# Kernel optimization log

Hardware: AMD Instinct MI355X
Metric: run time of the kernel (lower is better)

The kernel has to match this reference:

```python
import jax, jax.numpy as jnp
import numpy as np
from jax import lax

B, C, H, W = 8, 256, 128, 128
NH = 8
HD = C // NH
EPS = 1e-5


def setup_inputs() -> dict:
    key = jax.random.key(0)
    ks = jax.random.split(key, 6)
    x = jax.random.normal(ks[0], (B, C, H, W), dtype=jnp.float32)
    dw_weight = jax.random.normal(ks[1], (C, 1, 3, 3), dtype=jnp.float32) * 0.1
    off_weight = jax.random.normal(ks[2], (NH * 2, C), dtype=jnp.float32) * 0.05
    off_bias = jnp.zeros((NH * 2,), dtype=jnp.float32)
    v_weight = jax.random.normal(ks[3], (C, C), dtype=jnp.float32) * (1.0 / np.sqrt(C))
    o_weight = jax.random.normal(ks[4], (C, C), dtype=jnp.float32) * (1.0 / np.sqrt(C))
    gamma = jnp.ones((C,), dtype=jnp.float32)
    beta = jnp.zeros((C,), dtype=jnp.float32)
    return {"x": x, "dw_weight": dw_weight, "off_weight": off_weight, "off_bias": off_bias,
            "v_weight": v_weight, "o_weight": o_weight, "gamma": gamma, "beta": beta}


def reference(x, dw_weight, off_weight, off_bias, v_weight, o_weight, gamma, beta):
    b, c, h, w = x.shape
    # --- offset branch: depthwise 3x3 + pointwise 1x1 ---
    hdw = lax.conv_general_dilated(x, dw_weight, (1, 1), 'SAME',
                                   feature_group_count=c,
                                   dimension_numbers=('NCHW', 'OIHW', 'NCHW'))
    offsets = jnp.einsum('bchw,oc->bohw', hdw, off_weight) + off_bias[None, :, None, None]
    offsets = jnp.tanh(offsets) * 0.5                      # (B, 2*NH, H, W)
    offsets = offsets.reshape(b, NH, 2, h, w)
    dy, dx = offsets[:, :, 0], offsets[:, :, 1]            # (B, NH, H, W)

    # --- value projection, split into heads ---
    V = jnp.einsum('bchw,oc->bohw', x, v_weight).reshape(b, NH, HD, h, w)

    # --- deformable bilinear sampling (grid_sample, align_corners=True, border pad) ---
    gy = jnp.linspace(-1.0, 1.0, h, dtype=x.dtype)[None, None, :, None]
    gx = jnp.linspace(-1.0, 1.0, w, dtype=x.dtype)[None, None, None, :]
    sx = jnp.clip(gx + dx, -1.0, 1.0)                      # (B, NH, H, W)
    sy = jnp.clip(gy + dy, -1.0, 1.0)
    ix = (sx + 1.0) * 0.5 * (w - 1)                        # unnormalized coords
    iy = (sy + 1.0) * 0.5 * (h - 1)
    x0f = jnp.floor(ix); y0f = jnp.floor(iy)
    wx = ix - x0f; wy = iy - y0f
    x0 = jnp.clip(x0f.astype(jnp.int32), 0, w - 1)
    x1 = jnp.clip(x0f.astype(jnp.int32) + 1, 0, w - 1)
    y0 = jnp.clip(y0f.astype(jnp.int32), 0, h - 1)
    y1 = jnp.clip(y0f.astype(jnp.int32) + 1, 0, h - 1)

    Vf = V.reshape(b, NH, HD, h * w)

    def gather(yi, xi):
        idx = (yi * w + xi).reshape(b, NH, 1, h * w)
        return jnp.take_along_axis(Vf, idx, axis=3)        # (B, NH, HD, H*W)

    wx_ = wx.reshape(b, NH, 1, h * w); wy_ = wy.reshape(b, NH, 1, h * w)
    sampled = (gather(y0, x0) * (1 - wx_) * (1 - wy_)
               + gather(y0, x1) * wx_ * (1 - wy_)
               + gather(y1, x0) * (1 - wx_) * wy_
               + gather(y1, x1) * wx_ * wy_)
    out = sampled.reshape(b, c, h, w)

    # --- output projection + GroupNorm(NH groups) + residual ---
    out = jnp.einsum('bchw,oc->bohw', out, o_weight)
    g = out.reshape(b, NH, HD * h * w)
    mu = jnp.mean(g, axis=-1, keepdims=True)
    var = jnp.mean(jnp.square(g - mu), axis=-1, keepdims=True)
    g = (g - mu) * lax.rsqrt(var + EPS)
    out = g.reshape(b, c, h, w) * gamma[None, :, None, None] + beta[None, :, None, None]
    return x + out
```

## Files before the change

kernel.cpp:

```cpp
#include <hip/hip_runtime.h>
#include <hip/hip_bf16.h>

#define B_ 8
#define C_ 256
#define H_ 128
#define W_ 128
#define HW_ 16384
#define CHW_ (C_ * HW_)
#define NH_ 8
#define HD_ 32
#define NTOT (B_ * CHW_)

typedef short short8 __attribute__((ext_vector_type(8)));
typedef float f32x4 __attribute__((ext_vector_type(4)));

__global__ __launch_bounds__(256) void wconv_kernel(const float* __restrict__ vw,
                                                    const float* __restrict__ ow,
                                                    __hip_bfloat16* __restrict__ wvb,
                                                    __hip_bfloat16* __restrict__ wob) {
    int i = blockIdx.x * 256 + threadIdx.x;
    wvb[i] = __float2bfloat16(vw[i]);
    wob[i] = __float2bfloat16(ow[i]);
}

__global__ __launch_bounds__(256) void xt_kernel(const float* __restrict__ x,
                                                 __hip_bfloat16* __restrict__ xT) {
    __shared__ float tile[64][68];
    int t = threadIdx.x;
    int p0 = blockIdx.x * 64, c0 = blockIdx.y * 64, b = blockIdx.z;
    const float* xb = x + ((size_t)b * C_ + c0) * HW_ + p0;
#pragma unroll
    for (int l = 0; l < 4; ++l) {
        int idx = t + 256 * l;
        int row = idx >> 4, cf = idx & 15;
        float4 v = *(const float4*)&xb[(size_t)row * HW_ + cf * 4];
        *(float4*)&tile[row][cf * 4] = v;
    }
    __syncthreads();
    __hip_bfloat16* op = xT + ((size_t)b * HW_ + p0) * C_ + c0;
#pragma unroll
    for (int l = 0; l < 2; ++l) {
        int idx = t + 256 * l;
        int p = idx & 63, oct = idx >> 6;
        __hip_bfloat16 arr[8];
#pragma unroll
        for (int j = 0; j < 8; ++j) arr[j] = __float2bfloat16(tile[oct * 8 + j][p]);
        *(int4*)(op + (size_t)p * C_ + oct * 8) = *(int4*)arr;
    }
}

__global__ __launch_bounds__(256) void fused_offset_kernel(const float* __restrict__ x,
                                                           const float* __restrict__ dww,
                                                           const float* __restrict__ offw,
                                                           float* __restrict__ partials) {
    __shared__ float xt[4][10][136];
    __shared__ float wT[32][16];
    __shared__ float wd[32][9];
    int t = threadIdx.x;
    int rt = blockIdx.x, cg = blockIdx.y, b = blockIdx.z;
    int h0 = rt * 8, c0 = cg * 32;
    for (int i = t; i < 512; i += 256) { int o = i >> 5, c = i & 31; wT[c][o] = offw[o * 256 + c0 + c]; }
    for (int i = t; i < 288; i += 256) { wd[i / 9][i % 9] = dww[(c0 + i / 9) * 9 + i % 9]; }
    const float* xb = x + ((size_t)b * C_ + c0) * HW_;
    int col = t & 127;
    int sb = (t >> 7) * 4;
    float acc[4][16] = {};
    for (int cc0 = 0; cc0 < 32; cc0 += 4) {
        __syncthreads();
#pragma unroll
        for (int l = 0; l < 5; ++l) {
            int idx = t + 256 * l;
            int pr = idx >> 5, c4 = idx & 31;
            int cc = pr / 10, r = pr - cc * 10;
            int gh = h0 - 1 + r;
            float4 v = make_float4(0.f, 0.f, 0.f, 0.f);
            if (gh >= 0 && gh < H_)
                v = *(const float4*)&xb[(size_t)(cc0 + cc) * HW_ + gh * W_ + c4 * 4];
            *(float4*)&xt[cc][r][4 + c4 * 4] = v;
        }
        if (t < 80) { int pr = t >> 1, side = t & 1; xt[pr / 10][pr % 10][side ? 132 : 3] = 0.f; }
        __syncthreads();
#pragma unroll
        for (int cc = 0; cc < 4; ++cc) {
            float win[6][3];
#pragma unroll
            for (int rr = 0; rr < 6; ++rr)
#pragma unroll
                for (int kk = 0; kk < 3; ++kk)
                    win[rr][kk] = xt[cc][sb + rr][col + 3 + kk];
            float w9[9];
#pragma unroll
            for (int k9 = 0; k9 < 9; ++k9) w9[k9] = wd[cc0 + cc][k9];
#pragma unroll
            for (int j = 0; j < 4; ++j) {
                float s = 0.f;
#pragma unroll
                for (int ky = 0; ky < 3; ++ky)
#pragma unroll
                    for (int kx = 0; kx < 3; ++kx)
                        s += win[j + ky][kx] * w9[ky * 3 + kx];
#pragma unroll
                for (int o = 0; o < 16; ++o) acc[j][o] += s * wT[cc0 + cc][o];
            }
        }
    }
    float* pb = partials + (size_t)(cg * 8 + b) * 16 * HW_;
#pragma unroll
    for (int o = 0; o < 16; ++o)
#pragma unroll
        for (int j = 0; j < 4; ++j)
            pb[(size_t)o * HW_ + (h0 + sb + j) * W_ + col] = acc[j][o];
}

__global__ __launch_bounds__(256) void offreduce_kernel(const float* __restrict__ partials,
                                                        const float* __restrict__ offb,
                                                        float* __restrict__ off_buf) {
    int i = blockIdx.x * 256 + threadIdx.x;
    float s = 0.f;
#pragma unroll
    for (int cg = 0; cg < 8; ++cg) s += partials[(size_t)cg * 2097152 + i];
    int o = (i >> 14) & 15;
    off_buf[i] = tanhf(s + offb[o]) * 0.5f;
}

template<bool TRANS, bool STATS>
__global__ __launch_bounds__(256, 2) void mfma_gemm(const __hip_bfloat16* __restrict__ Wb,
                                                    const __hip_bfloat16* __restrict__ Xt,
                                                    void* __restrict__ Y,
                                                    float* __restrict__ stats) {
    int t = threadIdx.x;
    int wave = t >> 6, lane = t & 63;
    int quad = lane >> 4, l16 = lane & 15;
    int b = blockIdx.z;
    int n0 = blockIdx.x * 128, m0 = blockIdx.y * 128;
    const short* Wp = (const short*)Wb + (size_t)(m0 + wave * 32) * 256;
    const short* Xp = (const short*)Xt + ((size_t)b * HW_ + n0) * 256;

    short8 af[8][2];
#pragma unroll
    for (int ks = 0; ks < 8; ++ks)
#pragma unroll
        for (int mt = 0; mt < 2; ++mt)
            af[ks][mt] = *(const short8*)(Wp + (size_t)(mt * 16 + l16) * 256 + ks * 32 + quad * 8);

    const short* Xl = Xp + (size_t)l16 * 256 + quad * 8;
    short8 bf[3][8];
#pragma unroll
    for (int pf = 0; pf < 2; ++pf)
#pragma unroll
        for (int nt = 0; nt < 8; ++nt)
            bf[pf][nt] = *(const short8*)(Xl + (size_t)nt * 16 * 256 + pf * 32);

    f32x4 acc[2][8];
#pragma unroll
    for (int mt = 0; mt < 2; ++mt)
#pragma unroll
        for (int nt = 0; nt < 8; ++nt) acc[mt][nt] = (f32x4){0.f, 0.f, 0.f, 0.f};

#pragma unroll
    for (int ks = 0; ks < 8; ++ks) {
        if (ks < 6) {
#pragma unroll
            for (int nt = 0; nt < 8; ++nt)
                bf[(ks + 2) % 3][nt] = *(const short8*)(Xl + (size_t)nt * 16 * 256 + (ks + 2) * 32);
        }
#pragma unroll
        for (int mt = 0; mt < 2; ++mt)
#pragma unroll
            for (int nt = 0; nt < 8; ++nt)
                acc[mt][nt] = __builtin_amdgcn_mfma_f32_16x16x32_bf16(af[ks][mt], bf[ks % 3][nt], acc[mt][nt], 0, 0, 0);
    }

    if constexpr (TRANS) {
        __hip_bfloat16* Yb = (__hip_bfloat16*)Y + (size_t)b * CHW_;
#pragma unroll
        for (int mt = 0; mt < 2; ++mt)
#pragma unroll
            for (int nt = 0; nt < 8; ++nt) {
                int m = m0 + wave * 32 + mt * 16 + quad * 4;
                int n = n0 + nt * 16 + l16;
                __hip_bfloat16 arr[4];
#pragma unroll
                for (int r = 0; r < 4; ++r) arr[r] = __float2bfloat16(acc[mt][nt][r]);
                *(int2*)((__hip_bfloat16*)Yb + (size_t)n * C_ + m) = *(int2*)arr;
            }
    } else {
        float* Yb = (float*)Y + (size_t)b * CHW_;
#pragma unroll
        for (int mt = 0; mt < 2; ++mt)
#pragma unroll
            for (int nt = 0; nt < 8; ++nt)
#pragma unroll
                for (int r = 0; r < 4; ++r) {
                    int m = m0 + wave * 32 + mt * 16 + quad * 4 + r;
                    int n = n0 + nt * 16 + l16;
                    Yb[(size_t)m * HW_ + n] = acc[mt][nt][r];
                }
    }
    if constexpr (STATS) {
        float s1 = 0.f, s2 = 0.f;
#pragma unroll
        for (int mt = 0; mt < 2; ++mt)
#pragma unroll
            for (int nt = 0; nt < 8; ++nt)
#pragma unroll
                for (int r = 0; r < 4; ++r) {
                    float v = acc[mt][nt][r];
                    s1 += v;
                    s2 += v * v;
                }
#pragma unroll
        for (int o = 32; o; o >>= 1) {
            s1 += __shfl_down(s1, o);
            s2 += __shfl_down(s2, o);
        }
        if (lane == 0) {
            int grp = b * NH_ + (m0 >> 5) + wave;
            atomicAdd(&stats[grp * 2 + 0], s1);
            atomicAdd(&stats[grp * 2 + 1], s2);
        }
    }
}

__global__ __launch_bounds__(256) void sample_kernel(const __hip_bfloat16* __restrict__ VT,
                                                     const float* __restrict__ off,
                                                     __hip_bfloat16* __restrict__ sT) {
    int t = threadIdx.x;
    int chunk = t & 3;
    int g = t >> 2;
    int head = g & 7;
    int p = blockIdx.x * 8 + (g >> 3);
    int b = blockIdx.z;
    int h = p >> 7, w = p & 127;
    const float* ob = off + ((size_t)b * 16 + head * 2) * HW_ + p;
    float dy = ob[0], dx = ob[HW_];
    float gy = h * (2.0f / 127.0f) - 1.0f;
    float gx = w * (2.0f / 127.0f) - 1.0f;
    float sx = fminf(fmaxf(gx + dx, -1.0f), 1.0f);
    float sy = fminf(fmaxf(gy + dy, -1.0f), 1.0f);
    float ix = (sx + 1.0f) * 0.5f * 127.0f;
    float iy = (sy + 1.0f) * 0.5f * 127.0f;
    float x0f = floorf(ix), y0f = floorf(iy);
    float wx = ix - x0f, wy = iy - y0f;
    int x0 = min(max((int)x0f, 0), 127);
    int x1 = min((int)x0f + 1, 127);
    int y0 = min(max((int)y0f, 0), 127);
    int y1 = min((int)y0f + 1, 127);
    float w00 = (1.f - wx) * (1.f - wy), w01 = wx * (1.f - wy);
    float w10 = (1.f - wx) * wy, w11 = wx * wy;
    const short* Vb = (const short*)VT + (size_t)b * CHW_ + head * 32 + chunk * 8;
    short8 v00 = *(const short8*)(Vb + (size_t)(y0 * W_ + x0) * C_);
    short8 v01 = *(const short8*)(Vb + (size_t)(y0 * W_ + x1) * C_);
    short8 v10 = *(const short8*)(Vb + (size_t)(y1 * W_ + x0) * C_);
    short8 v11 = *(const short8*)(Vb + (size_t)(y1 * W_ + x1) * C_);
    __hip_bfloat16 arr[8];
#pragma unroll
    for (int j = 0; j < 8; ++j) {
        float f = __bfloat162float(((const __hip_bfloat16*)&v00)[j]) * w00 +
                  __bfloat162float(((const __hip_bfloat16*)&v01)[j]) * w01 +
                  __bfloat162float(((const __hip_bfloat16*)&v10)[j]) * w10 +
                  __bfloat162float(((const __hip_bfloat16*)&v11)[j]) * w11;
        arr[j] = __float2bfloat16(f);
    }
    __hip_bfloat16* op = sT + ((size_t)b * HW_ + p) * C_ + head * 32 + chunk * 8;
    *(int4*)op = *(int4*)arr;
}

__global__ __launch_bounds__(256) void final_kernel(const float* __restrict__ x,
                                                    const float* __restrict__ stats,
                                                    const float* __restrict__ gamma,
                                                    const float* __restrict__ beta,
                                                    float* __restrict__ out) {
    int idx = (blockIdx.x * 256 + threadIdx.x) * 4;
    int c = (idx >> 14) & 255;
    int b = idx >> 22;
    int grp = b * NH_ + (c >> 5);
    const float invN = 1.0f / (float)(HD_ * HW_);
    float mu = stats[grp * 2 + 0] * invN;
    float var = stats[grp * 2 + 1] * invN - mu * mu;
    float r = rsqrtf(var + 1e-5f);
    float g = gamma[c], be = beta[c];
    float4 v = *(const float4*)&out[idx];
    float4 xv = *(const float4*)&x[idx];
    float4 o;
    o.x = xv.x + (v.x - mu) * r * g + be;
    o.y = xv.y + (v.y - mu) * r * g + be;
    o.z = xv.z + (v.z - mu) * r * g + be;
    o.w = xv.w + (v.w - mu) * r * g + be;
    *(float4*)&out[idx] = o;
}

extern "C" void kernel_launch(void* const* d_in, const int* in_sizes, int n_in,
                              void* d_out, int out_size, void* d_ws, size_t ws_size,
                              hipStream_t stream) {
    const float* x     = (const float*)d_in[0];
    const float* dww   = (const float*)d_in[1];
    const float* offw  = (const float*)d_in[2];
    const float* offb  = (const float*)d_in[3];
    const float* vw    = (const float*)d_in[4];
    const float* ow    = (const float*)d_in[5];
    const float* gamma = (const float*)d_in[6];
    const float* beta  = (const float*)d_in[7];
    float* out = (float*)d_out;
    float* ws_f = (float*)d_ws;

    float* partials = ws_f;
    float* off_buf  = ws_f + 16777216;
    float* stats    = ws_f + 18874368;
    __hip_bfloat16* wvb = (__hip_bfloat16*)(ws_f + 18874624);
    __hip_bfloat16* wob = wvb + 65536;
    __hip_bfloat16* xT  = (__hip_bfloat16*)(ws_f + 18940160);
    __hip_bfloat16* sT  = (__hip_bfloat16*)partials;
    __hip_bfloat16* vT  = (__hip_bfloat16*)out;

    wconv_kernel<<<256, 256, 0, stream>>>(vw, ow, wvb, wob);
    xt_kernel<<<dim3(256, 4, 8), 256, 0, stream>>>(x, xT);
    fused_offset_kernel<<<dim3(16, 8, 8), 256, 0, stream>>>(x, dww, offw, partials);
    offreduce_kernel<<<8192, 256, 0, stream>>>(partials, offb, off_buf);
    mfma_gemm<true, false><<<dim3(128, 2, 8), 256, 0, stream>>>(wvb, xT, (void*)vT, nullptr);
    sample_kernel<<<dim3(2048, 1, 8), 256, 0, stream>>>(vT, off_buf, sT);
    hipMemsetAsync(stats, 0, 128 * sizeof(float), stream);
    mfma_gemm<false, true><<<dim3(128, 2, 8), 256, 0, stream>>>(wob, sT, (void*)out, stats);
    final_kernel<<<NTOT / 1024, 256, 0, stream>>>(x, stats, gamma, beta, out);
}
```

Before: 641.9 us.

## Stage GEMM tiles through swizzled LDS via global_load_lds with higher occupancy

The MFMA GEMM used to load A and B fragments straight from global memory into registers, with register double-buffering. It now copies 128x32 tiles of each operand into LDS with direct global-to-LDS loads, using an XOR swizzle to avoid bank conflicts. Fragments are then read from LDS, and each k-step is bracketed by barriers. Register use drops, so the launch bound rises to 4 blocks per CU, but the loads are no longer prefetched ahead of the compute and each step waits on two syncthreads.

Result: faster. 572.1 us (-10.9%).

```diff
diff --git a/kernel.cpp b/kernel.cpp
--- a/kernel.cpp
+++ b/kernel.cpp
@@ -124,51 +124,57 @@
 }
 
 template<bool TRANS, bool STATS>
-__global__ __launch_bounds__(256, 2) void mfma_gemm(const __hip_bfloat16* __restrict__ Wb,
+__global__ __launch_bounds__(256, 4) void mfma_gemm(const __hip_bfloat16* __restrict__ Wb,
                                                     const __hip_bfloat16* __restrict__ Xt,
                                                     void* __restrict__ Y,
                                                     float* __restrict__ stats) {
+    __shared__ __align__(16) short As[128 * 32];
+    __shared__ __align__(16) short Bs[128 * 32];
     int t = threadIdx.x;
     int wave = t >> 6, lane = t & 63;
     int quad = lane >> 4, l16 = lane & 15;
     int b = blockIdx.z;
     int n0 = blockIdx.x * 128, m0 = blockIdx.y * 128;
-    const short* Wp = (const short*)Wb + (size_t)(m0 + wave * 32) * 256;
+    const short* Wp = (const short*)Wb + (size_t)m0 * 256;
     const short* Xp = (const short*)Xt + ((size_t)b * HW_ + n0) * 256;
 
-    short8 af[8][2];
-#pragma unroll
-    for (int ks = 0; ks < 8; ++ks)
+    int i0 = t, i1 = t + 256;
+    int r0 = i0 >> 2, r1 = i1 >> 2;
+    int ss0 = (i0 & 3) ^ ((r0 >> 1) & 3);
+    int ss1 = (i1 & 3) ^ ((r1 >> 1) & 3);
+
+    f32x4 acc[2][8];
+#pragma unroll
+    for (int mt = 0; mt < 2; ++mt)
+#pragma unroll
+        for (int nt = 0; nt < 8; ++nt) acc[mt][nt] = (f32x4){0.f, 0.f, 0.f, 0.f};
+
+    for (int kk = 0; kk < 8; ++kk) {
+        int ko = kk * 32;
+        __builtin_amdgcn_global_load_lds(Wp + (size_t)r0 * 256 + ko + ss0 * 8, &As[i0 * 8], 16, 0, 0);
+        __builtin_amdgcn_global_load_lds(Wp + (size_t)r1 * 256 + ko + ss1 * 8, &As[i1 * 8], 16, 0, 0);
+        __builtin_amdgcn_global_load_lds(Xp + (size_t)r0 * 256 + ko + ss0 * 8, &Bs[i0 * 8], 16, 0, 0);
+        __builtin_amdgcn_global_load_lds(Xp + (size_t)r1 * 256 + ko + ss1 * 8, &Bs[i1 * 8], 16, 0, 0);
+        __syncthreads();
+        short8 af[2], bf[8];
+#pragma unroll
+        for (int mt = 0; mt < 2; ++mt) {
+            int r = wave * 32 + mt * 16 + l16;
+            int sl = quad ^ ((r >> 1) & 3);
+            af[mt] = *(const short8*)&As[r * 32 + sl * 8];
+        }
+#pragma unroll
+        for (int nt = 0; nt < 8; ++nt) {
+            int r = nt * 16 + l16;
+            int sl = quad ^ ((r >> 1) & 3);
+            bf[nt] = *(const short8*)&Bs[r * 32 + sl * 8];
+        }
 #pragma unroll
         for (int mt = 0; mt < 2; ++mt)
-            af[ks][mt] = *(const short8*)(Wp + (size_t)(mt * 16 + l16) * 256 + ks * 32 + quad * 8);
-
-    const short* Xl = Xp + (size_t)l16 * 256 + quad * 8;
-    short8 bf[3][8];
-#pragma unroll
-    for (int pf = 0; pf < 2; ++pf)
-#pragma unroll
-        for (int nt = 0; nt < 8; ++nt)
-            bf[pf][nt] = *(const short8*)(Xl + (size_t)nt * 16 * 256 + pf * 32);
-
-    f32x4 acc[2][8];
-#pragma unroll
-    for (int mt = 0; mt < 2; ++mt)
-#pragma unroll
-        for (int nt = 0; nt < 8; ++nt) acc[mt][nt] = (f32x4){0.f, 0.f, 0.f, 0.f};
-
-#pragma unroll
-    for (int ks = 0; ks < 8; ++ks) {
-        if (ks < 6) {
 #pragma unroll
             for (int nt = 0; nt < 8; ++nt)
-                bf[(ks + 2) % 3][nt] = *(const short8*)(Xl + (size_t)nt * 16 * 256 + (ks + 2) * 32);
-        }
-#pragma unroll
-        for (int mt = 0; mt < 2; ++mt)
-#pragma unroll
-            for (int nt = 0; nt < 8; ++nt)
-                acc[mt][nt] = __builtin_amdgcn_mfma_f32_16x16x32_bf16(af[ks][mt], bf[ks % 3][nt], acc[mt][nt], 0, 0, 0);
+                acc[mt][nt] = __builtin_amdgcn_mfma_f32_16x16x32_bf16(af[mt], bf[nt], acc[mt][nt], 0, 0, 0);
+        __syncthreads();
     }
 
     if constexpr (TRANS) {
```
